# Performance work log

Hardware: AMD Instinct MI355X
Metric: run time of the kernel (lower is better)

The kernel has to match this reference:

```python
import jax, jax.numpy as jnp
import numpy as np

IN_DIM = 4096
OUT_DIM = 4096
RANK = 8
IN1 = IN2 = OUT1 = OUT2 = 64  # factorize(4096) -> (64, 64)


def setup_inputs() -> dict:
    key = jax.random.key(0)
    k1, k2, k3, k4 = jax.random.split(key, 4)
    x = jax.random.normal(k1, (8, 2048, IN_DIM), dtype=jnp.float32)
    L = jax.random.normal(k2, (OUT1, OUT2, IN1, RANK), dtype=jnp.float32) * 0.05
    R = jax.random.normal(k3, (RANK, OUT2, IN1, IN2), dtype=jnp.float32) * 0.05
    bias = jax.random.normal(k4, (OUT_DIM,), dtype=jnp.float32) * 0.02
    return {"x": x, "L": L, "R": R, "bias": bias}


def reference(x, L, R, bias):
    # Assemble full weight: W[a,b,c,d] = sum_r L[a,b,c,r] * R[r,b,c,d]
    W = jnp.einsum('abcr,rbcd->abcd', L, R).reshape(OUT_DIM, IN_DIM)
    shape = x.shape
    X = x.reshape(-1, IN_DIM)          # [BS, in_dim]
    out = X @ W.T + bias               # addmm(bias, x, W.T)
    return out.reshape(*shape[:-1], OUT_DIM)
```

## Files before the change

### kernel.cpp

```cpp
#include <hip/hip_runtime.h>
#include <hip/hip_bf16.h>

typedef __attribute__((ext_vector_type(8))) short bf16x8;
typedef __attribute__((ext_vector_type(4))) float f32x4;

#define GLDS(g, l) \
  __builtin_amdgcn_global_load_lds((const __attribute__((address_space(1))) void*)(g), \
                                   (__attribute__((address_space(3))) void*)(l), 16, 0, 0)

#define MFMA_BF16 __builtin_amdgcn_mfma_f32_16x16x32_bf16

__global__ __launch_bounds__(256) void k_cvt_bf16(const float* __restrict__ x,
                                                  __hip_bfloat16* __restrict__ y,
                                                  long n8) {
  long stride = (long)gridDim.x * blockDim.x;
  for (long i = (long)blockIdx.x * blockDim.x + threadIdx.x; i < n8; i += stride) {
    const float4* xin = reinterpret_cast<const float4*>(x) + i * 2;
    float4 v0 = xin[0];
    float4 v1 = xin[1];
    union { __hip_bfloat16 h[8]; int4 v; } o;
    o.h[0] = __float2bfloat16(v0.x);
    o.h[1] = __float2bfloat16(v0.y);
    o.h[2] = __float2bfloat16(v0.z);
    o.h[3] = __float2bfloat16(v0.w);
    o.h[4] = __float2bfloat16(v1.x);
    o.h[5] = __float2bfloat16(v1.y);
    o.h[6] = __float2bfloat16(v1.z);
    o.h[7] = __float2bfloat16(v1.w);
    *reinterpret_cast<int4*>(y + i * 8) = o.v;
  }
}

__global__ __launch_bounds__(256) void k_make_w(const float* __restrict__ L,
                                                const float* __restrict__ R,
                                                __hip_bfloat16* __restrict__ W) {
  const int bc = blockIdx.x;
  const int b = bc >> 6, c = bc & 63;
  const int d = threadIdx.x & 63;
  const int q = threadIdx.x >> 6;
  float Rr[8];
#pragma unroll
  for (int r = 0; r < 8; ++r)
    Rr[r] = R[(((size_t)(r * 64 + b) * 64 + c) << 6) + d];
#pragma unroll 4
  for (int a = q * 16; a < q * 16 + 16; ++a) {
    const float* Lp = L + (((size_t)(a * 64 + b) * 64 + c) << 3);
    float s = 0.f;
#pragma unroll
    for (int r = 0; r < 8; ++r) s = fmaf(Lp[r], Rr[r], s);
    W[((size_t)(a * 64 + b) << 12) + (c << 6) + d] = __float2bfloat16(s);
  }
}

__global__ __launch_bounds__(512, 2) void k_gemm_bt(const __hip_bfloat16* __restrict__ A,
                                                    const __hip_bfloat16* __restrict__ B,
                                                    const float* __restrict__ bias,
                                                    float* __restrict__ C) {
  const int K = 4096, N = 4096, NT = 64;
  __shared__ char lds[131072];
  char* const sAc = lds;
  char* const sBc = lds + 65536;

  const int tid = threadIdx.x;
  const int lane = tid & 63;
  const int wid = tid >> 6;
  const int wr = wid >> 2;
  const int wc = wid & 3;

  const int orig = blockIdx.x;
  const int wg = (orig & 7) * 128 + (orig >> 3);
  const int gm0 = (wg >> 4) * 256;
  const int gn0 = (wg & 15) * 256;

  const int crow = tid >> 3;
  const int scol = ((tid & 7) << 4) ^ ((crow & 7) << 4);
  const int voff = crow * 8192 + scol;
  const int wbase = (tid >> 6) << 10;
  const char* const Ab = (const char*)(A + (size_t)gm0 * K);
  const char* const Bb = (const char*)(B + (size_t)gn0 * K);

#define STAGEA(BUF, TS)                                                      \
  _Pragma("unroll")                                                          \
  for (int j = 0; j < 4; ++j)                                                \
    GLDS(Ab + (size_t)((TS) * 128 + j * 524288) + voff,                      \
         sAc + (BUF) * 32768 + j * 8192 + wbase);

#define STAGEB(BUF, TS)                                                      \
  _Pragma("unroll")                                                          \
  for (int j = 0; j < 4; ++j)                                                \
    GLDS(Bb + (size_t)((TS) * 128 + j * 524288) + voff,                      \
         sBc + (BUF) * 32768 + j * 8192 + wbase);

  const int lr = lane & 15;
  const int lk = lane >> 4;
  const int kx0 = (lk << 4) ^ ((lr & 7) << 4);
  const int kx1 = (64 + (lk << 4)) ^ ((lr & 7) << 4);
  const char* const rA0 = sAc + (((wr << 7) + lr) << 7) + kx0;
  const char* const rA1 = sAc + (((wr << 7) + lr) << 7) + kx1;
  const char* const rB0 = sBc + (((wc << 6) + lr) << 7) + kx0;
  const char* const rB1 = sBc + (((wc << 6) + lr) << 7) + kx1;

#define PREFA(DST, BUF, MOFS)                                                \
  _Pragma("unroll")                                                          \
  for (int m = 0; m < 4; ++m) {                                              \
    DST[m][0] = *(const bf16x8*)(rA0 + (BUF) * 32768 + ((MOFS) + m) * 2048); \
    DST[m][1] = *(const bf16x8*)(rA1 + (BUF) * 32768 + ((MOFS) + m) * 2048); \
  }

#define PREFB(DST, BUF, NOFS)                                                \
  _Pragma("unroll")                                                          \
  for (int n = 0; n < 2; ++n) {                                              \
    DST[n][0] = *(const bf16x8*)(rB0 + (BUF) * 32768 + ((NOFS) + n) * 2048); \
    DST[n][1] = *(const bf16x8*)(rB1 + (BUF) * 32768 + ((NOFS) + n) * 2048); \
  }

#define MFMA8X(AF, BF, MB, NB)                                               \
  _Pragma("unroll")                                                          \
  for (int m = 0; m < 4; ++m) {                                              \
    acc[(MB) + m][(NB) + 0] =                                                \
        MFMA_BF16(AF[m][0], BF[0][0], acc[(MB) + m][(NB) + 0], 0, 0, 0);     \
    acc[(MB) + m][(NB) + 0] =                                                \
        MFMA_BF16(AF[m][1], BF[0][1], acc[(MB) + m][(NB) + 0], 0, 0, 0);     \
    acc[(MB) + m][(NB) + 1] =                                                \
        MFMA_BF16(AF[m][0], BF[1][0], acc[(MB) + m][(NB) + 1], 0, 0, 0);     \
    acc[(MB) + m][(NB) + 1] =                                                \
        MFMA_BF16(AF[m][1], BF[1][1], acc[(MB) + m][(NB) + 1], 0, 0, 0);     \
  }

#define LGKM0 asm volatile("s_waitcnt lgkmcnt(0)" ::: "memory")
#define SBAR0 __builtin_amdgcn_sched_barrier(0)

  const int er = gm0 + (wr << 7) + ((lane >> 4) << 2);
  const int ec = gn0 + (wc << 6) + (lane & 15);

  f32x4 acc[8][4];
#pragma unroll
  for (int n = 0; n < 4; ++n) {
    const float bv = bias[ec + n * 16];
#pragma unroll
    for (int m = 0; m < 8; ++m) acc[m][n] = (f32x4){bv, bv, bv, bv};
  }

  bf16x8 aX[4][2], aY[4][2], b0[2][2], b2[2][2];

  STAGEA(0, 0) STAGEB(0, 0) STAGEA(1, 1) STAGEB(1, 1)
  asm volatile("s_waitcnt vmcnt(8)" ::: "memory");
  SBAR0;
  __builtin_amdgcn_s_barrier();
  PREFA(aX, 0, 0) PREFB(b0, 0, 0)

#define TILE(BUF, T)                                                         \
  {                                                                          \
    const int tS = ((T) + 2 < NT) ? (T) + 2 : NT - 1;                        \
                                                                     \
    LGKM0; SBAR0;                                                            \
    PREFA(aY, BUF, 4)                                                        \
    SBAR0;                                                                   \
    __builtin_amdgcn_s_setprio(1);                                           \
    MFMA8X(aX, b0, 0, 0)                                                     \
    __builtin_amdgcn_s_setprio(0);                                           \
                                                                     \
    LGKM0; SBAR0;                                                            \
    PREFB(b2, BUF, 2)                                                        \
    SBAR0;                                                                   \
    __builtin_amdgcn_s_setprio(1);                                           \
    MFMA8X(aY, b0, 4, 0)                                                     \
    __builtin_amdgcn_s_setprio(0);                                           \
     \
    asm volatile("s_waitcnt lgkmcnt(0) vmcnt(0)" ::: "memory");              \
    SBAR0;                                                                   \
    __builtin_amdgcn_s_barrier();                                            \
    STAGEA(BUF, tS)                                                          \
    PREFB(b0, (BUF) ^ 1, 0)                                                  \
    SBAR0;                                                                   \
    __builtin_amdgcn_s_setprio(1);                                           \
    MFMA8X(aX, b2, 0, 2)                                                     \
    __builtin_amdgcn_s_setprio(0);                                           \
                                           \
    SBAR0;                                                                   \
    STAGEB(BUF, tS)                                                          \
    PREFA(aX, (BUF) ^ 1, 0)                                                  \
    SBAR0;                                                                   \
    __builtin_amdgcn_s_setprio(1);                                           \
    MFMA8X(aY, b2, 4, 2)                                                     \
    __builtin_amdgcn_s_setprio(0);                                           \
  }

  for (int t = 0; t < NT; t += 2) {
    TILE(0, t)
    TILE(1, t + 1)
  }
  asm volatile("s_waitcnt vmcnt(0) lgkmcnt(0)" ::: "memory");

#pragma unroll
  for (int n = 0; n < 4; ++n) {
    const int c = ec + n * 16;
#pragma unroll
    for (int m = 0; m < 8; ++m) {
#pragma unroll
      for (int j = 0; j < 4; ++j) {
        C[(size_t)(er + m * 16 + j) * N + c] = acc[m][n][j];
      }
    }
  }
}

extern "C" void kernel_launch(void* const* d_in, const int* in_sizes, int n_in,
                              void* d_out, int out_size, void* d_ws, size_t ws_size,
                              hipStream_t stream) {
  const float* x = (const float*)d_in[0];
  const float* L = (const float*)d_in[1];
  const float* R = (const float*)d_in[2];
  const float* bias = (const float*)d_in[3];
  float* out = (float*)d_out;

  __hip_bfloat16* Wb = (__hip_bfloat16*)d_ws;
  __hip_bfloat16* Xb = (__hip_bfloat16*)((char*)d_ws + (size_t)4096 * 4096 * 2);

  const long n8 = (long)16384 * 4096 / 8;
  k_cvt_bf16<<<4096, 256, 0, stream>>>(x, Xb, n8);
  k_make_w<<<4096, 256, 0, stream>>>(L, R, Wb);

  dim3 grid(1024);
  k_gemm_bt<<<grid, 512, 0, stream>>>(Xb, Wb, bias, out);
}
```

Before: 569.6 us.

## Load GEMM B operand directly from global into registers, merge prep kernels

Merges the x-to-bf16 conversion and weight assembly into one launch with a block-index split. In the GEMM, the B (weight) tile is no longer staged through LDS; each wave loads its B fragments from global memory straight into double-buffered registers one tile ahead. This halves LDS use, which may allow more resident blocks, and removes the B LDS writes and reads. The cost is uncoalesced 16-byte global loads for B, reuse of B across the two wave rows only through cache, more registers, and vmcnt accounting that has to match the issue order exactly.

```diff
diff --git a/kernel.cpp b/kernel.cpp
--- a/kernel.cpp
+++ b/kernel.cpp
@@ -10,45 +10,46 @@
 
 #define MFMA_BF16 __builtin_amdgcn_mfma_f32_16x16x32_bf16
 
-__global__ __launch_bounds__(256) void k_cvt_bf16(const float* __restrict__ x,
-                                                  __hip_bfloat16* __restrict__ y,
-                                                  long n8) {
-  long stride = (long)gridDim.x * blockDim.x;
-  for (long i = (long)blockIdx.x * blockDim.x + threadIdx.x; i < n8; i += stride) {
-    const float4* xin = reinterpret_cast<const float4*>(x) + i * 2;
-    float4 v0 = xin[0];
-    float4 v1 = xin[1];
-    union { __hip_bfloat16 h[8]; int4 v; } o;
-    o.h[0] = __float2bfloat16(v0.x);
-    o.h[1] = __float2bfloat16(v0.y);
-    o.h[2] = __float2bfloat16(v0.z);
-    o.h[3] = __float2bfloat16(v0.w);
-    o.h[4] = __float2bfloat16(v1.x);
-    o.h[5] = __float2bfloat16(v1.y);
-    o.h[6] = __float2bfloat16(v1.z);
-    o.h[7] = __float2bfloat16(v1.w);
-    *reinterpret_cast<int4*>(y + i * 8) = o.v;
-  }
-}
-
-__global__ __launch_bounds__(256) void k_make_w(const float* __restrict__ L,
-                                                const float* __restrict__ R,
-                                                __hip_bfloat16* __restrict__ W) {
-  const int bc = blockIdx.x;
-  const int b = bc >> 6, c = bc & 63;
-  const int d = threadIdx.x & 63;
-  const int q = threadIdx.x >> 6;
-  float Rr[8];
-#pragma unroll
-  for (int r = 0; r < 8; ++r)
-    Rr[r] = R[(((size_t)(r * 64 + b) * 64 + c) << 6) + d];
+__global__ __launch_bounds__(256) void k_prep(const float* __restrict__ x,
+                                              __hip_bfloat16* __restrict__ y,
+                                              const float* __restrict__ L,
+                                              const float* __restrict__ R,
+                                              __hip_bfloat16* __restrict__ W) {
+  if (blockIdx.x < 4096) {
+    const long n8 = (long)16384 * 4096 / 8;
+    const long stride = (long)4096 * 256;
+    for (long i = (long)blockIdx.x * 256 + threadIdx.x; i < n8; i += stride) {
+      const float4* xin = reinterpret_cast<const float4*>(x) + i * 2;
+      float4 v0 = xin[0];
+      float4 v1 = xin[1];
+      union { __hip_bfloat16 h[8]; int4 v; } o;
+      o.h[0] = __float2bfloat16(v0.x);
+      o.h[1] = __float2bfloat16(v0.y);
+      o.h[2] = __float2bfloat16(v0.z);
+      o.h[3] = __float2bfloat16(v0.w);
+      o.h[4] = __float2bfloat16(v1.x);
+      o.h[5] = __float2bfloat16(v1.y);
+      o.h[6] = __float2bfloat16(v1.z);
+      o.h[7] = __float2bfloat16(v1.w);
+      *reinterpret_cast<int4*>(y + i * 8) = o.v;
+    }
+  } else {
+    const int bc = blockIdx.x - 4096;
+    const int b = bc >> 6, c = bc & 63;
+    const int d = threadIdx.x & 63;
+    const int q = threadIdx.x >> 6;
+    float Rr[8];
+#pragma unroll
+    for (int r = 0; r < 8; ++r)
+      Rr[r] = R[(((size_t)(r * 64 + b) * 64 + c) << 6) + d];
 #pragma unroll 4
-  for (int a = q * 16; a < q * 16 + 16; ++a) {
-    const float* Lp = L + (((size_t)(a * 64 + b) * 64 + c) << 3);
-    float s = 0.f;
-#pragma unroll
-    for (int r = 0; r < 8; ++r) s = fmaf(Lp[r], Rr[r], s);
-    W[((size_t)(a * 64 + b) << 12) + (c << 6) + d] = __float2bfloat16(s);
+    for (int a = q * 16; a < q * 16 + 16; ++a) {
+      const float* Lp = L + (((size_t)(a * 64 + b) * 64 + c) << 3);
+      float s = 0.f;
+#pragma unroll
+      for (int r = 0; r < 8; ++r) s = fmaf(Lp[r], Rr[r], s);
+      W[((size_t)(a * 64 + b) << 12) + (c << 6) + d] = __float2bfloat16(s);
+    }
   }
 }
 
@@ -57,9 +58,8 @@
                                                     const float* __restrict__ bias,
                                                     float* __restrict__ C) {
   const int K = 4096, N = 4096, NT = 64;
-  __shared__ char lds[131072];
+  __shared__ char lds[65536];
   char* const sAc = lds;
-  char* const sBc = lds + 65536;
 
   const int tid = threadIdx.x;
   const int lane = tid & 63;
@@ -77,19 +77,12 @@
   const int voff = crow * 8192 + scol;
   const int wbase = (tid >> 6) << 10;
   const char* const Ab = (const char*)(A + (size_t)gm0 * K);
-  const char* const Bb = (const char*)(B + (size_t)gn0 * K);
 
 #define STAGEA(BUF, TS)                                                      \
   _Pragma("unroll")                                                          \
   for (int j = 0; j < 4; ++j)                                                \
     GLDS(Ab + (size_t)((TS) * 128 + j * 524288) + voff,                      \
          sAc + (BUF) * 32768 + j * 8192 + wbase);
-
-#define STAGEB(BUF, TS)                                                      \
-  _Pragma("unroll")                                                          \
-  for (int j = 0; j < 4; ++j)                                                \
-    GLDS(Bb + (size_t)((TS) * 128 + j * 524288) + voff,                      \
-         sBc + (BUF) * 32768 + j * 8192 + wbase);
 
   const int lr = lane & 15;
   const int lk = lane >> 4;
@@ -97,8 +90,6 @@
   const int kx1 = (64 + (lk << 4)) ^ ((lr & 7) << 4);
   const char* const rA0 = sAc + (((wr << 7) + lr) << 7) + kx0;
   const char* const rA1 = sAc + (((wr << 7) + lr) << 7) + kx1;
-  const char* const rB0 = sBc + (((wc << 6) + lr) << 7) + kx0;
-  const char* const rB1 = sBc + (((wc << 6) + lr) << 7) + kx1;
 
 #define PREFA(DST, BUF, MOFS)                                                \
   _Pragma("unroll")                                                          \
@@ -107,12 +98,21 @@
     DST[m][1] = *(const bf16x8*)(rA1 + (BUF) * 32768 + ((MOFS) + m) * 2048); \
   }
 
-#define PREFB(DST, BUF, NOFS)                                                \
-  _Pragma("unroll")                                                          \
-  for (int n = 0; n < 2; ++n) {                                              \
-    DST[n][0] = *(const bf16x8*)(rB0 + (BUF) * 32768 + ((NOFS) + n) * 2048); \
-    DST[n][1] = *(const bf16x8*)(rB1 + (BUF) * 32768 + ((NOFS) + n) * 2048); \
-  }
+  const char* const Bq = (const char*)(B + (size_t)gn0 * K) +
+                         (size_t)((wc << 6) + lr) * 8192 + (lk << 4);
+
+#define LOADB01K0(BN, TB)                                                    \
+  BN##01[0][0] = *(const bf16x8*)(Bq + (size_t)(TB) * 128);                  \
+  BN##01[1][0] = *(const bf16x8*)(Bq + 131072 + (size_t)(TB) * 128);
+#define LOADB01K1(BN, TB)                                                    \
+  BN##01[0][1] = *(const bf16x8*)(Bq + (size_t)(TB) * 128 + 64);             \
+  BN##01[1][1] = *(const bf16x8*)(Bq + 131072 + (size_t)(TB) * 128 + 64);
+#define LOADB23K0(BN, TB)                                                    \
+  BN##23[0][0] = *(const bf16x8*)(Bq + 262144 + (size_t)(TB) * 128);         \
+  BN##23[1][0] = *(const bf16x8*)(Bq + 393216 + (size_t)(TB) * 128);
+#define LOADB23K1(BN, TB)                                                    \
+  BN##23[0][1] = *(const bf16x8*)(Bq + 262144 + (size_t)(TB) * 128 + 64);    \
+  BN##23[1][1] = *(const bf16x8*)(Bq + 393216 + (size_t)(TB) * 128 + 64);
 
 #define MFMA8X(AF, BF, MB, NB)                                               \
   _Pragma("unroll")                                                          \
@@ -129,6 +129,7 @@
 
 #define LGKM0 asm volatile("s_waitcnt lgkmcnt(0)" ::: "memory")
 #define SBAR0 __builtin_amdgcn_sched_barrier(0)
+#define VMC(N) asm volatile("s_waitcnt vmcnt(" #N ")" ::: "memory")
 
   const int er = gm0 + (wr << 7) + ((lane >> 4) << 2);
   const int ec = gn0 + (wc << 6) + (lane & 15);
@@ -141,54 +142,60 @@
     for (int m = 0; m < 8; ++m) acc[m][n] = (f32x4){bv, bv, bv, bv};
   }
 
-  bf16x8 aX[4][2], aY[4][2], b0[2][2], b2[2][2];
-
-  STAGEA(0, 0) STAGEB(0, 0) STAGEA(1, 1) STAGEB(1, 1)
-  asm volatile("s_waitcnt vmcnt(8)" ::: "memory");
+  bf16x8 aX[4][2], aY[4][2];
+  bf16x8 bA01[2][2], bA23[2][2], bB01[2][2], bB23[2][2];
+
+  STAGEA(0, 0)
+  LOADB01K0(bA, 0) LOADB01K1(bA, 0)
+  STAGEA(1, 1)
+  LOADB23K0(bA, 0) LOADB23K1(bA, 0)
+  VMC(12);
   SBAR0;
   __builtin_amdgcn_s_barrier();
-  PREFA(aX, 0, 0) PREFB(b0, 0, 0)
-
-#define TILE(BUF, T)                                                         \
+  PREFA(aX, 0, 0)
+
+#define TILE(BUF, BC, BN, T)                                                 \
   {                                                                          \
     const int tS = ((T) + 2 < NT) ? (T) + 2 : NT - 1;                        \
-                                                                     \
+    const int tB = ((T) + 1 < NT) ? (T) + 1 : NT - 1;                        \
+                                                     \
+    VMC(8); SBAR0;                                                           \
     LGKM0; SBAR0;                                                            \
     PREFA(aY, BUF, 4)                                                        \
-    SBAR0;                                                                   \
-    __builtin_amdgcn_s_setprio(1);                                           \
-    MFMA8X(aX, b0, 0, 0)                                                     \
-    __builtin_amdgcn_s_setprio(0);                                           \
-                                                                     \
+    LOADB01K0(BN, tB)                                                        \
+    SBAR0;                                                                   \
+    __builtin_amdgcn_s_setprio(1);                                           \
+    MFMA8X(aX, BC##01, 0, 0)                                                 \
+    __builtin_amdgcn_s_setprio(0);                                           \
+                                                     \
     LGKM0; SBAR0;                                                            \
-    PREFB(b2, BUF, 2)                                                        \
-    SBAR0;                                                                   \
-    __builtin_amdgcn_s_setprio(1);                                           \
-    MFMA8X(aY, b0, 4, 0)                                                     \
-    __builtin_amdgcn_s_setprio(0);                                           \
-     \
-    asm volatile("s_waitcnt lgkmcnt(0) vmcnt(0)" ::: "memory");              \
-    SBAR0;                                                                   \
+    LOADB01K1(BN, tB)                                                        \
+    SBAR0;                                                                   \
+    __builtin_amdgcn_s_setprio(1);                                           \
+    MFMA8X(aY, BC##01, 4, 0)                                                 \
+    __builtin_amdgcn_s_setprio(0);                                           \
+           \
+    VMC(8); SBAR0;                                                           \
     __builtin_amdgcn_s_barrier();                                            \
     STAGEA(BUF, tS)                                                          \
-    PREFB(b0, (BUF) ^ 1, 0)                                                  \
-    SBAR0;                                                                   \
-    __builtin_amdgcn_s_setprio(1);                                           \
-    MFMA8X(aX, b2, 0, 2)                                                     \
-    __builtin_amdgcn_s_setprio(0);                                           \
-                                           \
-    SBAR0;                                                                   \
-    STAGEB(BUF, tS)                                                          \
+    LOADB23K0(BN, tB)                                                        \
+    VMC(10); SBAR0;                                                          \
+    __builtin_amdgcn_s_setprio(1);                                           \
+    MFMA8X(aX, BC##23, 0, 2)                                                 \
+    __builtin_amdgcn_s_setprio(0);                                           \
+                                                     \
+    SBAR0;                                                                   \
     PREFA(aX, (BUF) ^ 1, 0)                                                  \
-    SBAR0;                                                                   \
-    __builtin_amdgcn_s_setprio(1);                                           \
-    MFMA8X(aY, b2, 4, 2)                                                     \
+    LOADB23K1(BN, tB)                                                        \
+    SBAR0;                                                                   \
+    __builtin_amdgcn_s_setprio(1);                                           \
+    MFMA8X(aY, BC##23, 4, 2)                                                 \
     __builtin_amdgcn_s_setprio(0);                                           \
   }
 
   for (int t = 0; t < NT; t += 2) {
-    TILE(0, t)
-    TILE(1, t + 1)
+    TILE(0, bA, bB, t)
+    TILE(1, bB, bA, t + 1)
   }
   asm volatile("s_waitcnt vmcnt(0) lgkmcnt(0)" ::: "memory");
 
@@ -217,9 +224,7 @@
   __hip_bfloat16* Wb = (__hip_bfloat16*)d_ws;
   __hip_bfloat16* Xb = (__hip_bfloat16*)((char*)d_ws + (size_t)4096 * 4096 * 2);
 
-  const long n8 = (long)16384 * 4096 / 8;
-  k_cvt_bf16<<<4096, 256, 0, stream>>>(x, Xb, n8);
-  k_make_w<<<4096, 256, 0, stream>>>(L, R, Wb);
+  k_prep<<<8192, 256, 0, stream>>>(x, Xb, L, R, Wb);
 
   dim3 grid(1024);
   k_gemm_bt<<<grid, 512, 0, stream>>>(Xb, Wb, bias, out);
```

New measurement: 1.207 ms. 112% more time.
